# Performance work log

Hardware: AMD Instinct MI355X
Metric: run time of the kernel (lower is better)

## Reference

```python
import jax, jax.numpy as jnp
import numpy as np

D_MODEL = 128; N_HEADS = 4; N_LAYERS = 6
D_STATE = 16; D_CONV = 4; EXPAND = 2
D_INNER = EXPAND * D_MODEL          # 256
DT_RANK = (D_MODEL + 15) // 16      # 8
MLP_HID = 32
B, L = 8, 2048


def _ln(x, s, b):
    m = jnp.mean(x, -1, keepdims=True)
    v = jnp.var(x, -1, keepdims=True)
    return (x - m) / jnp.sqrt(v + 1e-5) * s + b


def _pe(length, d):
    # standard sinusoidal positional encoding [length, d]
    pos = jnp.arange(length, dtype=jnp.float32)[:, None]
    div = jnp.exp(jnp.arange(0, d, 2, dtype=jnp.float32) * (-np.log(10000.0) / d))
    pe = jnp.zeros((length, d), dtype=jnp.float32)
    pe = pe.at[:, 0::2].set(jnp.sin(pos * div))
    pe = pe.at[:, 1::2].set(jnp.cos(pos * div))
    return pe


def setup_inputs() -> dict:
    ks = iter(jax.random.split(jax.random.key(0), 48))
    def p(shape, scale=0.02):
        return jax.random.normal(next(ks), shape, dtype=jnp.float32) * scale
    return dict(
        x=jax.random.normal(next(ks), (B, L, 1), dtype=jnp.float32),
        mlp1_w=p((D_MODEL, 1)), mlp1_b=p((D_MODEL,)),
        qkv_w=p((N_LAYERS, 3 * D_MODEL, D_MODEL)), qkv_b=p((N_LAYERS, 3 * D_MODEL)),
        attn_out_w=p((N_LAYERS, D_MODEL, D_MODEL)), attn_out_b=p((N_LAYERS, D_MODEL)),
        ln1_s=jnp.ones((N_LAYERS, D_MODEL)), ln1_b=jnp.zeros((N_LAYERS, D_MODEL)),
        ffw_w1=p((N_LAYERS, D_MODEL, D_MODEL)), ffw_b1=p((N_LAYERS, D_MODEL)),
        ffw_w2=p((N_LAYERS, D_MODEL, D_MODEL)), ffw_b2=p((N_LAYERS, D_MODEL)),
        ln2_s=jnp.ones((N_LAYERS, D_MODEL)), ln2_b=jnp.zeros((N_LAYERS, D_MODEL)),
        in_proj_w=p((2 * D_INNER, D_MODEL)),
        conv_w=p((D_INNER, 1, D_CONV)), conv_b=p((D_INNER,)),
        x_proj_w=p((DT_RANK + 2 * D_STATE, D_INNER)),
        dt_proj_w=p((D_INNER, DT_RANK)), dt_proj_b=p((D_INNER,)),
        A_log=jnp.log(jnp.tile(jnp.arange(1, D_STATE + 1, dtype=jnp.float32), (D_INNER, 1))),
        D_skip=jnp.ones((D_INNER,), dtype=jnp.float32),
        out_proj_w=p((D_MODEL, D_INNER)),
        mlp2_w1=p((MLP_HID, D_MODEL)), mlp2_b1=p((MLP_HID,)),
        mlp2_w2=p((1, MLP_HID)), mlp2_b2=p((1,)),
    )


def _forward(x, mlp1_w, mlp1_b, qkv_w, qkv_b, attn_out_w, attn_out_b,
             ln1_s, ln1_b, ffw_w1, ffw_b1, ffw_w2, ffw_b2, ln2_s, ln2_b,
             in_proj_w, conv_w, conv_b, x_proj_w, dt_proj_w, dt_proj_b,
             A_log, D_skip, out_proj_w, mlp2_w1, mlp2_b1, mlp2_w2, mlp2_b2):
    b, l, _ = x.shape
    dh = D_MODEL // N_HEADS
    # mlp1 + positional encoding (dropout is identity at eval)
    h = x @ mlp1_w.T + mlp1_b                       # [B,L,D]
    h = h + _pe(l, D_MODEL)[None]
    # 6 post-norm self-attention + FFW layers (query_pos=None -> plain MHA)
    for i in range(N_LAYERS):
        qkv = h @ qkv_w[i].T + qkv_b[i]
        q, k, v = jnp.split(qkv, 3, axis=-1)
        q = q.reshape(b, l, N_HEADS, dh); k = k.reshape(b, l, N_HEADS, dh)
        v = v.reshape(b, l, N_HEADS, dh)
        scores = jnp.einsum('blhd,bmhd->bhlm', q, k) / jnp.sqrt(jnp.float32(dh))
        attn = jax.nn.softmax(scores, axis=-1)
        o = jnp.einsum('bhlm,bmhd->blhd', attn, v).reshape(b, l, D_MODEL)
        o = o @ attn_out_w[i].T + attn_out_b[i]
        h = _ln(h + o, ln1_s[i], ln1_b[i])
        f = jax.nn.relu(h @ ffw_w1[i].T + ffw_b1[i]) @ ffw_w2[i].T + ffw_b2[i]
        h = _ln(h + f, ln2_s[i], ln2_b[i])
    # Mamba block
    xz = h @ in_proj_w.T                            # [B,L,2*Din]
    xm, z = jnp.split(xz, 2, axis=-1)
    xc = xm.transpose(0, 2, 1)                      # [B,Din,L]
    xc = jax.lax.conv_general_dilated(
        xc, conv_w, (1,), [(D_CONV - 1, 0)],
        feature_group_count=D_INNER, dimension_numbers=('NCH', 'OIH', 'NCH'))
    xc = xc + conv_b[None, :, None]
    xm = jax.nn.silu(xc.transpose(0, 2, 1))         # [B,L,Din]
    dbc = xm @ x_proj_w.T                           # [B,L,dt_rank+2S]
    dt, Bm, Cm = jnp.split(dbc, [DT_RANK, DT_RANK + D_STATE], axis=-1)
    dt = jax.nn.softplus(dt @ dt_proj_w.T + dt_proj_b)  # [B,L,Din]
    A = -jnp.exp(A_log)                             # [Din,S]
    dA = jnp.exp(jnp.einsum('bld,ds->blds', dt, A))     # [B,L,Din,S]
    dBx = jnp.einsum('bld,bls,bld->blds', dt, Bm, xm)   # [B,L,Din,S]

    def step(hstate, inp):
        dA_t, dBx_t, C_t = inp
        hstate = hstate * dA_t + dBx_t             # [B,Din,S]
        y = jnp.einsum('bds,bs->bd', hstate, C_t)
        return hstate, y

    h0 = jnp.zeros((b, D_INNER, D_STATE), dtype=xm.dtype)
    _, ys = jax.lax.scan(step, h0, (dA.transpose(1, 0, 2, 3),
                                    dBx.transpose(1, 0, 2, 3),
                                    Cm.transpose(1, 0, 2)))
    y = ys.transpose(1, 0, 2)                       # [B,L,Din]
    y = y + xm * D_skip
    y = y * jax.nn.silu(z)
    y = y @ out_proj_w.T                            # [B,L,D]
    pooled = jnp.mean(y, axis=1)                    # [B,D]
    out = jax.nn.relu(pooled @ mlp2_w1.T + mlp2_b1) @ mlp2_w2.T + mlp2_b2
    return out                                      # [B,1]


def reference(x, mlp1_w, mlp1_b, qkv_w, qkv_b, attn_out_w, attn_out_b,
              ln1_s, ln1_b, ffw_w1, ffw_b1, ffw_w2, ffw_b2, ln2_s, ln2_b,
              in_proj_w, conv_w, conv_b, x_proj_w, dt_proj_w, dt_proj_b,
              A_log, D_skip, out_proj_w, mlp2_w1, mlp2_b1, mlp2_w2, mlp2_b2):
    return _forward(x, mlp1_w, mlp1_b, qkv_w, qkv_b, attn_out_w, attn_out_b,
                    ln1_s, ln1_b, ffw_w1, ffw_b1, ffw_w2, ffw_b2, ln2_s, ln2_b,
                    in_proj_w, conv_w, conv_b, x_proj_w, dt_proj_w, dt_proj_b,
                    A_log, D_skip, out_proj_w, mlp2_w1, mlp2_b1, mlp2_w2, mlp2_b2)
```

## Files before the change

### kernel.cpp

```cpp
#include <hip/hip_runtime.h>
#include <math.h>

#define BB 8
#define LL 2048
#define DMODEL 128
#define NHEAD 4
#define DHEAD 32
#define DIN 256
#define DSTATE 16
#define NLAYERS 6
#define BLROWS (BB*LL)
#define NCHUNK 32
#define CH 64

typedef __attribute__((ext_vector_type(8))) short short8;
typedef __attribute__((ext_vector_type(4))) float f32x4;

static __device__ __forceinline__ unsigned cvt_pk_bf16(float a, float b) {
    unsigned r;
    asm volatile("v_cvt_pk_bf16_f32 %0, %1, %2" : "=v"(r) : "v"(a), "v"(b));
    return r;
}
static __device__ __forceinline__ float fexp2(float x) {
    float r;
    asm("v_exp_f32 %0, %1" : "=v"(r) : "v"(x));
    return r;
}

__global__ __launch_bounds__(256) void wcvt_k(
    const float* __restrict__ src, ushort* __restrict__ dst, int n4)
{
    int i = blockIdx.x * 256 + threadIdx.x;
    if (i < n4) {
        float4 v = ((const float4*)src)[i];
        uint2 pw; pw.x = cvt_pk_bf16(v.x, v.y); pw.y = cvt_pk_bf16(v.z, v.w);
        ((uint2*)dst)[i] = pw;
    }
}

__global__ __launch_bounds__(256) void mlp1_pe_k(
    const float* __restrict__ x, const float* __restrict__ w,
    const float* __restrict__ b, float* __restrict__ h)
{
    int idx = blockIdx.x * 256 + threadIdx.x;
    int d   = idx & 127;
    int row = idx >> 7;
    int pos = row & (LL - 1);
    float v = x[row] * w[d] + b[d];
    int j2 = (d >> 1) * 2;
    float dv = expf((float)j2 * -0.07195578415603638f);
    float ang = (float)pos * dv;
    v += (d & 1) ? cosf(ang) : sinf(ang);
    h[idx] = v;
}

#define QSCALE (0.17677669529663687f * 1.4426950408889634f)
__global__ __launch_bounds__(256) void gemm_qkv_k(
    const float* __restrict__ A, const ushort* __restrict__ W16,
    const float* __restrict__ bias, ushort* __restrict__ C16)
{
    __shared__ __align__(16) short As[64][136];
    __shared__ __align__(16) short Ws[128][136];
    int tid = threadIdx.x;
    int w = tid >> 6, lane = tid & 63, lg = lane >> 4, lr = lane & 15;
    int row0 = blockIdx.y * 64, col0 = blockIdx.x * 128;

    const float* Ab = A + (size_t)row0 * 128;
    #pragma unroll
    for (int p = 0; p < 8; ++p) {
        int off = p * 1024 + tid * 4;
        float4 v = *(const float4*)(Ab + off);
        uint2 pw; pw.x = cvt_pk_bf16(v.x, v.y); pw.y = cvt_pk_bf16(v.z, v.w);
        *(uint2*)&As[off >> 7][off & 127] = pw;
    }
    const ushort* Wb = W16 + (size_t)col0 * 128;
    #pragma unroll
    for (int p = 0; p < 8; ++p) {
        int off = p * 2048 + tid * 8;
        short8 v = *(const short8*)(Wb + off);
        *(short8*)&Ws[off >> 7][off & 127] = v;
    }
    __syncthreads();

    short8 af[4];
    #pragma unroll
    for (int kk = 0; kk < 4; ++kk)
        af[kk] = *(short8*)&As[w * 16 + lr][kk * 32 + lg * 8];
    f32x4 acc[8];
    #pragma unroll
    for (int n = 0; n < 8; ++n) acc[n] = (f32x4){0.f, 0.f, 0.f, 0.f};
    #pragma unroll
    for (int n = 0; n < 8; ++n)
        #pragma unroll
        for (int kk = 0; kk < 4; ++kk) {
            short8 bf = *(short8*)&Ws[n * 16 + lr][kk * 32 + lg * 8];
            acc[n] = __builtin_amdgcn_mfma_f32_16x16x32_bf16(af[kk], bf, acc[n], 0, 0, 0);
        }
    float qs = (blockIdx.x == 0) ? QSCALE : 1.f;
    #pragma unroll
    for (int n = 0; n < 8; ++n) {
        int col = col0 + n * 16 + lr;
        float bv = bias[col];
        #pragma unroll
        for (int j = 0; j < 4; ++j) {
            int row = row0 + w * 16 + lg * 4 + j;
            float v = (acc[n][j] + bv) * qs;
            C16[(size_t)row * 384 + col] = (ushort)cvt_pk_bf16(v, v);
        }
    }
}

__global__ __launch_bounds__(256) void gemm_bf16_k(
    const float* __restrict__ A, const ushort* __restrict__ W16,
    float* __restrict__ C, int N)
{
    __shared__ __align__(16) short As[64][136];
    __shared__ __align__(16) short Ws[128][136];
    int tid = threadIdx.x;
    int w = tid >> 6, lane = tid & 63, lg = lane >> 4, lr = lane & 15;
    int row0 = blockIdx.y * 64, col0 = blockIdx.x * 128;

    const float* Ab = A + (size_t)row0 * 128;
    #pragma unroll
    for (int p = 0; p < 8; ++p) {
        int off = p * 1024 + tid * 4;
        float4 v = *(const float4*)(Ab + off);
        uint2 pw; pw.x = cvt_pk_bf16(v.x, v.y); pw.y = cvt_pk_bf16(v.z, v.w);
        *(uint2*)&As[off >> 7][off & 127] = pw;
    }
    const ushort* Wb = W16 + (size_t)col0 * 128;
    #pragma unroll
    for (int p = 0; p < 8; ++p) {
        int off = p * 2048 + tid * 8;
        short8 v = *(const short8*)(Wb + off);
        *(short8*)&Ws[off >> 7][off & 127] = v;
    }
    __syncthreads();

    short8 af[4];
    #pragma unroll
    for (int kk = 0; kk < 4; ++kk)
        af[kk] = *(short8*)&As[w * 16 + lr][kk * 32 + lg * 8];
    f32x4 acc[8];
    #pragma unroll
    for (int n = 0; n < 8; ++n) acc[n] = (f32x4){0.f, 0.f, 0.f, 0.f};
    #pragma unroll
    for (int n = 0; n < 8; ++n)
        #pragma unroll
        for (int kk = 0; kk < 4; ++kk) {
            short8 bf = *(short8*)&Ws[n * 16 + lr][kk * 32 + lg * 8];
            acc[n] = __builtin_amdgcn_mfma_f32_16x16x32_bf16(af[kk], bf, acc[n], 0, 0, 0);
        }
    #pragma unroll
    for (int n = 0; n < 8; ++n) {
        int col = col0 + n * 16 + lr;
        #pragma unroll
        for (int j = 0; j < 4; ++j) {
            int row = row0 + w * 16 + lg * 4 + j;
            C[(size_t)row * N + col] = acc[n][j];
        }
    }
}

__global__ __launch_bounds__(256) void gemm_ln_k(
    const ushort* __restrict__ A16, const ushort* __restrict__ W16,
    const float* __restrict__ bias, float* __restrict__ h,
    const float* __restrict__ ls, const float* __restrict__ lb)
{
    __shared__ __align__(16) short As[64][136];
    __shared__ __align__(16) short Ws[128][136];
    int tid = threadIdx.x;
    int w = tid >> 6, lane = tid & 63, lg = lane >> 4, lr = lane & 15;
    int row0 = blockIdx.x * 64;

    const ushort* Ab = A16 + (size_t)row0 * 128;
    #pragma unroll
    for (int p = 0; p < 4; ++p) {
        int off = p * 2048 + tid * 8;
        short8 v = *(const short8*)(Ab + off);
        *(short8*)&As[off >> 7][off & 127] = v;
    }
    #pragma unroll
    for (int p = 0; p < 8; ++p) {
        int off = p * 2048 + tid * 8;
        short8 v = *(const short8*)(W16 + off);
        *(short8*)&Ws[off >> 7][off & 127] = v;
    }
    __syncthreads();

    short8 af[4];
    #pragma unroll
    for (int kk = 0; kk < 4; ++kk)
        af[kk] = *(short8*)&As[w * 16 + lr][kk * 32 + lg * 8];
    f32x4 acc[8];
    #pragma unroll
    for (int n = 0; n < 8; ++n) acc[n] = (f32x4){0.f, 0.f, 0.f, 0.f};
    #pragma unroll
    for (int n = 0; n < 8; ++n)
        #pragma unroll
        for (int kk = 0; kk < 4; ++kk) {
            short8 bf = *(short8*)&Ws[n * 16 + lr][kk * 32 + lg * 8];
            acc[n] = __builtin_amdgcn_mfma_f32_16x16x32_bf16(af[kk], bf, acc[n], 0, 0, 0);
        }

    float bv[8], lsv[8], lbv[8];
    #pragma unroll
    for (int n = 0; n < 8; ++n) {
        int col = n * 16 + lr;
        bv[n] = bias[col]; lsv[n] = ls[col]; lbv[n] = lb[col];
    }
    #pragma unroll
    for (int j = 0; j < 4; ++j) {
        int row = row0 + w * 16 + lg * 4 + j;
        float xv[8]; float sum = 0.f;
        #pragma unroll
        for (int n = 0; n < 8; ++n) {
            xv[n] = acc[n][j] + bv[n] + h[(size_t)row * 128 + n * 16 + lr];
            sum += xv[n];
        }
        sum += __shfl_xor(sum, 1); sum += __shfl_xor(sum, 2);
        sum += __shfl_xor(sum, 4); sum += __shfl_xor(sum, 8);
        float mean = sum * (1.f / 128.f);
        float vs = 0.f;
        #pragma unroll
        for (int n = 0; n < 8; ++n) { float dd = xv[n] - mean; vs += dd * dd; }
        vs += __shfl_xor(vs, 1); vs += __shfl_xor(vs, 2);
        vs += __shfl_xor(vs, 4); vs += __shfl_xor(vs, 8);
        float inv = rsqrtf(vs * (1.f / 128.f) + 1e-5f);
        #pragma unroll
        for (int n = 0; n < 8; ++n)
            h[(size_t)row * 128 + n * 16 + lr] = (xv[n] - mean) * inv * lsv[n] + lbv[n];
    }
}

__global__ __launch_bounds__(256) void ffw_ln_k(
    float* __restrict__ h, const ushort* __restrict__ W1, const float* __restrict__ b1,
    const ushort* __restrict__ W2, const float* __restrict__ b2,
    const float* __restrict__ ls, const float* __restrict__ lb)
{
    __shared__ __align__(16) short As[64][136];
    __shared__ __align__(16) short Ws[128][136];
    int tid = threadIdx.x;
    int w = tid >> 6, lane = tid & 63, lg = lane >> 4, lr = lane & 15;
    int row0 = blockIdx.x * 64;

    const float* Ab = h + (size_t)row0 * 128;
    #pragma unroll
    for (int p = 0; p < 8; ++p) {
        int off = p * 1024 + tid * 4;
        float4 v = *(const float4*)(Ab + off);
        uint2 pw; pw.x = cvt_pk_bf16(v.x, v.y); pw.y = cvt_pk_bf16(v.z, v.w);
        *(uint2*)&As[off >> 7][off & 127] = pw;
    }
    #pragma unroll
    for (int p = 0; p < 8; ++p) {
        int off = p * 2048 + tid * 8;
        short8 v = *(const short8*)(W1 + off);
        *(short8*)&Ws[off >> 7][off & 127] = v;
    }
    __syncthreads();

    short8 af[4];
    #pragma unroll
    for (int kk = 0; kk < 4; ++kk)
        af[kk] = *(short8*)&As[w * 16 + lr][kk * 32 + lg * 8];
    f32x4 acc[8];
    #pragma unroll
    for (int n = 0; n < 8; ++n) acc[n] = (f32x4){0.f, 0.f, 0.f, 0.f};
    #pragma unroll
    for (int n = 0; n < 8; ++n)
        #pragma unroll
        for (int kk = 0; kk < 4; ++kk) {
            short8 bf = *(short8*)&Ws[n * 16 + lr][kk * 32 + lg * 8];
            acc[n] = __builtin_amdgcn_mfma_f32_16x16x32_bf16(af[kk], bf, acc[n], 0, 0, 0);
        }
    __syncthreads();

    {
        float b1v[8];
        #pragma unroll
        for (int n = 0; n < 8; ++n) b1v[n] = b1[n * 16 + lr];
        #pragma unroll
        for (int n = 0; n < 8; ++n) {
            #pragma unroll
            for (int j = 0; j < 4; ++j) {
                float hv = fmaxf(acc[n][j] + b1v[n], 0.f);
                As[w * 16 + lg * 4 + j][n * 16 + lr] = (short)cvt_pk_bf16(hv, hv);
            }
        }
    }
    #pragma unroll
    for (int p = 0; p < 8; ++p) {
        int off = p * 2048 + tid * 8;
        short8 v = *(const short8*)(W2 + off);
        *(short8*)&Ws[off >> 7][off & 127] = v;
    }
    __syncthreads();

    #pragma unroll
    for (int kk = 0; kk < 4; ++kk)
        af[kk] = *(short8*)&As[w * 16 + lr][kk * 32 + lg * 8];
    #pragma unroll
    for (int n = 0; n < 8; ++n) acc[n] = (f32x4){0.f, 0.f, 0.f, 0.f};
    #pragma unroll
    for (int n = 0; n < 8; ++n)
        #pragma unroll
        for (int kk = 0; kk < 4; ++kk) {
            short8 bf = *(short8*)&Ws[n * 16 + lr][kk * 32 + lg * 8];
            acc[n] = __builtin_amdgcn_mfma_f32_16x16x32_bf16(af[kk], bf, acc[n], 0, 0, 0);
        }

    float bv[8], lsv[8], lbv[8];
    #pragma unroll
    for (int n = 0; n < 8; ++n) {
        int col = n * 16 + lr;
        bv[n] = b2[col]; lsv[n] = ls[col]; lbv[n] = lb[col];
    }
    #pragma unroll
    for (int j = 0; j < 4; ++j) {
        int row = row0 + w * 16 + lg * 4 + j;
        float xv[8]; float sum = 0.f;
        #pragma unroll
        for (int n = 0; n < 8; ++n) {
            xv[n] = acc[n][j] + bv[n] + h[(size_t)row * 128 + n * 16 + lr];
            sum += xv[n];
        }
        sum += __shfl_xor(sum, 1); sum += __shfl_xor(sum, 2);
        sum += __shfl_xor(sum, 4); sum += __shfl_xor(sum, 8);
        float mean = sum * (1.f / 128.f);
        float vs = 0.f;
        #pragma unroll
        for (int n = 0; n < 8; ++n) { float dd = xv[n] - mean; vs += dd * dd; }
        vs += __shfl_xor(vs, 1); vs += __shfl_xor(vs, 2);
        vs += __shfl_xor(vs, 4); vs += __shfl_xor(vs, 8);
        float inv = rsqrtf(vs * (1.f / 128.f) + 1e-5f);
        #pragma unroll
        for (int n = 0; n < 8; ++n)
            h[(size_t)row * 128 + n * 16 + lr] = (xv[n] - mean) * inv * lsv[n] + lbv[n];
    }
}

__global__ __launch_bounds__(256) void attn_mfma_k(
    const ushort* __restrict__ qkv, ushort* __restrict__ o)
{
    __shared__ __align__(16) char smem[16384];

    int bid = blockIdx.x;
    int b  = bid & 7;
    int qt = (bid >> 3) & 15;
    int hd = bid >> 7;
    int tid  = threadIdx.x;
    int wave = tid >> 6;
    int lane = tid & 63;
    int lg = lane >> 4, lr = lane & 15;

    const ushort* base = qkv + (size_t)b * LL * 384;
    int qr0 = qt * 128 + wave * 32;

    short8 qfA = *(const short8*)(base + (size_t)(qr0 + lr) * 384 + hd * 32 + lg * 8);
    short8 qfB = *(const short8*)(base + (size_t)(qr0 + 16 + lr) * 384 + hd * 32 + lg * 8);

    int kk = tid >> 2, ks = tid & 3;
    int krow = kk & 31;
    int kchk = (((kk >> 5) << 2) + ks) ^ (krow & 7);
    int kwo = krow * 128 + (kchk << 4);
    const ushort* kptr = base + (size_t)kk * 384 + 128 + hd * 32 + ks * 8;

    int k2 = (tid & 31) * 2, d0 = (tid >> 5) * 4;
    int rl = k2 & 31;
    int colp = (k2 >> 5) * 32 + ((rl >> 2) & 3) * 8 + (rl >> 4) * 4 + (rl & 3);
    int vchunk = colp >> 3;
    int vinb   = (colp * 2) & 15;
    int vwo0 = (d0+0)*128 + (((vchunk ^ ((d0+0)&7)) << 4) | vinb);
    int vwo1 = (d0+1)*128 + (((vchunk ^ ((d0+1)&7)) << 4) | vinb);
    int vwo2 = (d0+2)*128 + (((vchunk ^ ((d0+2)&7)) << 4) | vinb);
    int vwo3 = (d0+3)*128 + (((vchunk ^ ((d0+3)&7)) << 4) | vinb);
    const ushort* vptr = base + (size_t)k2 * 384 + 256 + hd * 32 + d0;

    int kro[4];
    #pragma unroll
    for (int n = 0; n < 4; ++n) {
        int r = ((n & 1) << 4) + lr;
        int c = (((n >> 1) << 2) + lg) ^ (r & 7);
        kro[n] = r * 128 + (c << 4);
    }
    int sx = (lg ^ (lr & 7)) << 4;
    int sy = ((4 + lg) ^ (lr & 7)) << 4;
    int vro0 = lr * 128 + sx;
    int vro1 = (16 + lr) * 128 + sx;
    int vro2 = lr * 128 + sy;
    int vro3 = (16 + lr) * 128 + sy;

    f32x4 OfA[2] = {}, OfB[2] = {};
    f32x4 OlA = {}, OlB = {};
    const f32x4 zero4 = {0.f, 0.f, 0.f, 0.f};
    short8 ones;
    #pragma unroll
    for (int e = 0; e < 8; ++e) ones[e] = (short)0x3F80;

    const int TSTR = 64 * 384;
    const ushort* knext = kptr;
    const ushort* vnext = vptr;

    {
        short8 kreg = *(const short8*)knext;
        uint2 va = *(const uint2*)vnext;
        uint2 vb = *(const uint2*)(vnext + 384);
        knext += TSTR; vnext += TSTR;
        *(short8*)(smem + 0 + kwo) = kreg;
        uint w0 = (va.x & 0xFFFFu) | (vb.x << 16);
        uint w1 = (va.x >> 16)     | (vb.x & 0xFFFF0000u);
        uint w2 = (va.y & 0xFFFFu) | (vb.y << 16);
        uint w3 = (va.y >> 16)     | (vb.y & 0xFFFF0000u);
        *(uint*)(smem + 8192 + vwo0) = w0;
        *(uint*)(smem + 8192 + vwo1) = w1;
        *(uint*)(smem + 8192 + vwo2) = w2;
        *(uint*)(smem + 8192 + vwo3) = w3;
    }
    __syncthreads();

#define ATTN_TILE(KRB, VRB, KWB, VWB, LAST) do {                              \
    short8 kreg_; uint2 va_, vb_;                                             \
    if (!(LAST)) {                                                            \
        kreg_ = *(const short8*)knext;                                        \
        va_   = *(const uint2*)vnext;                                         \
        vb_   = *(const uint2*)(vnext + 384);                                 \
        knext += TSTR; vnext += TSTR;                                         \
    }                                                                         \
    short8 kf0_ = *(const short8*)(smem + (KRB) + kro[0]);                    \
    short8 kf1_ = *(const short8*)(smem + (KRB) + kro[1]);                    \
    short8 kf2_ = *(const short8*)(smem + (KRB) + kro[2]);                    \
    short8 kf3_ = *(const short8*)(smem + (KRB) + kro[3]);                    \
    f32x4 SA0_ = __builtin_amdgcn_mfma_f32_16x16x32_bf16(kf0_, qfA, zero4,0,0,0); \
    f32x4 SA1_ = __builtin_amdgcn_mfma_f32_16x16x32_bf16(kf1_, qfA, zero4,0,0,0); \
    f32x4 SA2_ = __builtin_amdgcn_mfma_f32_16x16x32_bf16(kf2_, qfA, zero4,0,0,0); \
    f32x4 SA3_ = __builtin_amdgcn_mfma_f32_16x16x32_bf16(kf3_, qfA, zero4,0,0,0); \
    f32x4 SB0_ = __builtin_amdgcn_mfma_f32_16x16x32_bf16(kf0_, qfB, zero4,0,0,0); \
    f32x4 SB1_ = __builtin_amdgcn_mfma_f32_16x16x32_bf16(kf1_, qfB, zero4,0,0,0); \
    f32x4 SB2_ = __builtin_amdgcn_mfma_f32_16x16x32_bf16(kf2_, qfB, zero4,0,0,0); \
    f32x4 SB3_ = __builtin_amdgcn_mfma_f32_16x16x32_bf16(kf3_, qfB, zero4,0,0,0); \
    union { uint4 u; short8 s; } paA0_, paA1_, paB0_, paB1_;                  \
    paA0_.u.x = cvt_pk_bf16(fexp2(SA0_[0]), fexp2(SA0_[1]));                  \
    paA0_.u.y = cvt_pk_bf16(fexp2(SA0_[2]), fexp2(SA0_[3]));                  \
    paA0_.u.z = cvt_pk_bf16(fexp2(SA1_[0]), fexp2(SA1_[1]));                  \
    paA0_.u.w = cvt_pk_bf16(fexp2(SA1_[2]), fexp2(SA1_[3]));                  \
    paA1_.u.x = cvt_pk_bf16(fexp2(SA2_[0]), fexp2(SA2_[1]));                  \
    paA1_.u.y = cvt_pk_bf16(fexp2(SA2_[2]), fexp2(SA2_[3]));                  \
    paA1_.u.z = cvt_pk_bf16(fexp2(SA3_[0]), fexp2(SA3_[1]));                  \
    paA1_.u.w = cvt_pk_bf16(fexp2(SA3_[2]), fexp2(SA3_[3]));                  \
    paB0_.u.x = cvt_pk_bf16(fexp2(SB0_[0]), fexp2(SB0_[1]));                  \
    paB0_.u.y = cvt_pk_bf16(fexp2(SB0_[2]), fexp2(SB0_[3]));                  \
    paB0_.u.z = cvt_pk_bf16(fexp2(SB1_[0]), fexp2(SB1_[1]));                  \
    paB0_.u.w = cvt_pk_bf16(fexp2(SB1_[2]), fexp2(SB1_[3]));                  \
    paB1_.u.x = cvt_pk_bf16(fexp2(SB2_[0]), fexp2(SB2_[1]));                  \
    paB1_.u.y = cvt_pk_bf16(fexp2(SB2_[2]), fexp2(SB2_[3]));                  \
    paB1_.u.z = cvt_pk_bf16(fexp2(SB3_[0]), fexp2(SB3_[1]));                  \
    paB1_.u.w = cvt_pk_bf16(fexp2(SB3_[2]), fexp2(SB3_[3]));                  \
    short8 vb00_ = *(const short8*)(smem + (VRB) + vro0);                     \
    short8 vb01_ = *(const short8*)(smem + (VRB) + vro1);                     \
    short8 vb10_ = *(const short8*)(smem + (VRB) + vro2);                     \
    short8 vb11_ = *(const short8*)(smem + (VRB) + vro3);                     \
    OlA    = __builtin_amdgcn_mfma_f32_16x16x32_bf16(paA0_.s, ones,  OlA,   0,0,0); \
    OfA[0] = __builtin_amdgcn_mfma_f32_16x16x32_bf16(paA0_.s, vb00_, OfA[0],0,0,0); \
    OfA[1] = __builtin_amdgcn_mfma_f32_16x16x32_bf16(paA0_.s, vb01_, OfA[1],0,0,0); \
    OlA    = __builtin_amdgcn_mfma_f32_16x16x32_bf16(paA1_.s, ones,  OlA,   0,0,0); \
    OfA[0] = __builtin_amdgcn_mfma_f32_16x16x32_bf16(paA1_.s, vb10_, OfA[0],0,0,0); \
    OfA[1] = __builtin_amdgcn_mfma_f32_16x16x32_bf16(paA1_.s, vb11_, OfA[1],0,0,0); \
    OlB    = __builtin_amdgcn_mfma_f32_16x16x32_bf16(paB0_.s, ones,  OlB,   0,0,0); \
    OfB[0] = __builtin_amdgcn_mfma_f32_16x16x32_bf16(paB0_.s, vb00_, OfB[0],0,0,0); \
    OfB[1] = __builtin_amdgcn_mfma_f32_16x16x32_bf16(paB0_.s, vb01_, OfB[1],0,0,0); \
    OlB    = __builtin_amdgcn_mfma_f32_16x16x32_bf16(paB1_.s, ones,  OlB,   0,0,0); \
    OfB[0] = __builtin_amdgcn_mfma_f32_16x16x32_bf16(paB1_.s, vb10_, OfB[0],0,0,0); \
    OfB[1] = __builtin_amdgcn_mfma_f32_16x16x32_bf16(paB1_.s, vb11_, OfB[1],0,0,0); \
    if (!(LAST)) {                                                            \
        *(short8*)(smem + (KWB) + kwo) = kreg_;                               \
        uint w0_ = (va_.x & 0xFFFFu) | (vb_.x << 16);                         \
        uint w1_ = (va_.x >> 16)     | (vb_.x & 0xFFFF0000u);                 \
        uint w2_ = (va_.y & 0xFFFFu) | (vb_.y << 16);                         \
        uint w3_ = (va_.y >> 16)     | (vb_.y & 0xFFFF0000u);                 \
        *(uint*)(smem + (VWB) + vwo0) = w0_;                                  \
        *(uint*)(smem + (VWB) + vwo1) = w1_;                                  \
        *(uint*)(smem + (VWB) + vwo2) = w2_;                                  \
        *(uint*)(smem + (VWB) + vwo3) = w3_;                                  \
    }                                                                         \
    __syncthreads();                                                          \
} while (0)

    #pragma unroll 1
    for (int t = 0; t < 32; t += 2) {
        ATTN_TILE(0,    8192,  4096, 12288, false);
        ATTN_TILE(4096, 12288, 0,    8192,  (t + 2 >= 32));
    }
#undef ATTN_TILE

    #pragma unroll
    for (int j = 0; j < 4; ++j) {
        float invA = 1.f / OlA[j];
        int qA = qr0 + lg * 4 + j;
        size_t obA = ((size_t)b * LL + qA) * DMODEL + hd * 32;
        float a0 = OfA[0][j] * invA, a1 = OfA[1][j] * invA;
        o[obA + lr]      = (ushort)cvt_pk_bf16(a0, a0);
        o[obA + 16 + lr] = (ushort)cvt_pk_bf16(a1, a1);
        float invB = 1.f / OlB[j];
        int qB = qr0 + 16 + lg * 4 + j;
        size_t obB = ((size_t)b * LL + qB) * DMODEL + hd * 32;
        float b0 = OfB[0][j] * invB, b1 = OfB[1][j] * invB;
        o[obB + lr]      = (ushort)cvt_pk_bf16(b0, b0);
        o[obB + 16 + lr] = (ushort)cvt_pk_bf16(b1, b1);
    }
}

__global__ __launch_bounds__(256) void xproj_bf16_k(
    const float* __restrict__ A, const ushort* __restrict__ W16,
    float* __restrict__ C)
{
    __shared__ __align__(16) short As[64][264];
    __shared__ __align__(16) short Ws[48][264];
    int tid = threadIdx.x;
    int w = tid >> 6, lane = tid & 63, lg = lane >> 4, lr = lane & 15;
    int row0 = blockIdx.x * 64;

    const float* Ab = A + (size_t)row0 * 256;
    #pragma unroll
    for (int p = 0; p < 16; ++p) {
        int off = p * 1024 + tid * 4;
        float4 v = *(const float4*)(Ab + off);
        uint2 pw; pw.x = cvt_pk_bf16(v.x, v.y); pw.y = cvt_pk_bf16(v.z, v.w);
        *(uint2*)&As[off >> 8][off & 255] = pw;
    }
    #pragma unroll
    for (int p = 0; p < 6; ++p) {
        int off = p * 2048 + tid * 8;
        int r = off >> 8, c = off & 255;
        short8 v = {};
        if (r < 40) v = *(const short8*)(W16 + (size_t)r * 256 + c);
        *(short8*)&Ws[r][c] = v;
    }
    __syncthreads();

    short8 af[8];
    #pragma unroll
    for (int kk = 0; kk < 8; ++kk)
        af[kk] = *(short8*)&As[w * 16 + lr][kk * 32 + lg * 8];

    f32x4 acc[3];
    #pragma unroll
    for (int n = 0; n < 3; ++n) acc[n] = (f32x4){0.f, 0.f, 0.f, 0.f};
    #pragma unroll
    for (int n = 0; n < 3; ++n)
        #pragma unroll
        for (int kk = 0; kk < 8; ++kk) {
            short8 bf = *(short8*)&Ws[n * 16 + lr][kk * 32 + lg * 8];
            acc[n] = __builtin_amdgcn_mfma_f32_16x16x32_bf16(af[kk], bf, acc[n], 0, 0, 0);
        }
    #pragma unroll
    for (int n = 0; n < 3; ++n) {
        int col = n * 16 + lr;
        if (col < 40) {
            #pragma unroll
            for (int j = 0; j < 4; ++j) {
                int row = row0 + w * 16 + lg * 4 + j;
                C[(size_t)row * 40 + col] = acc[n][j];
            }
        }
    }
}

__global__ __launch_bounds__(256) void conv_silu_k(
    const float* __restrict__ xz, const float* __restrict__ cw,
    const float* __restrict__ cb, float* __restrict__ xm)
{
    int idx = blockIdx.x * 256 + threadIdx.x;
    int d   = idx & 255;
    int row = idx >> 8;
    int l   = row & (LL - 1);
    float a = cb[d];
    #pragma unroll
    for (int t = 0; t < 4; ++t) {
        int ll = l - 3 + t;
        if (ll >= 0) a += cw[d * 4 + t] * xz[(size_t)(row - 3 + t) * 512 + d];
    }
    float sg = 1.f / (1.f + expf(-a));
    xm[idx] = a * sg;
}

__global__ __launch_bounds__(256) void dtproj_k(
    const float* __restrict__ dbc, const float* __restrict__ w,
    const float* __restrict__ bias, float* __restrict__ dt)
{
    int row0 = blockIdx.x * 4, n = threadIdx.x;
    __shared__ float dv[4][8];
    if (n < 32) dv[n >> 3][n & 7] = dbc[(size_t)(row0 + (n >> 3)) * 40 + (n & 7)];
    __syncthreads();
    float bv = bias[n];
    float wv[8];
    #pragma unroll
    for (int k = 0; k < 8; ++k) wv[k] = w[n * 8 + k];
    #pragma unroll
    for (int r = 0; r < 4; ++r) {
        float a = bv;
        #pragma unroll
        for (int k = 0; k < 8; ++k) a += dv[r][k] * wv[k];
        float sp = fmaxf(a, 0.f) + log1pf(expf(-fabsf(a)));
        dt[(size_t)(row0 + r) * 256 + n] = sp;
    }
}

__global__ __launch_bounds__(512) void scan1_k(
    const float* __restrict__ dt, const float* __restrict__ xm,
    const float* __restrict__ dbc, const float* __restrict__ A_log,
    float* __restrict__ Asum, float* __restrict__ Bsum)
{
    int blk = blockIdx.x;
    int c = blk & 31, b = blk >> 5;
    int tid = threadIdx.x;
    int d = tid >> 1, sh = tid & 1;
    float Av2[8];
    {
        float4 a0 = *(const float4*)(A_log + d * 16 + sh * 8);
        float4 a1 = *(const float4*)(A_log + d * 16 + sh * 8 + 4);
        Av2[0] = -expf(a0.x) * 1.4426950408889634f;
        Av2[1] = -expf(a0.y) * 1.4426950408889634f;
        Av2[2] = -expf(a0.z) * 1.4426950408889634f;
        Av2[3] = -expf(a0.w) * 1.4426950408889634f;
        Av2[4] = -expf(a1.x) * 1.4426950408889634f;
        Av2[5] = -expf(a1.y) * 1.4426950408889634f;
        Av2[6] = -expf(a1.z) * 1.4426950408889634f;
        Av2[7] = -expf(a1.w) * 1.4426950408889634f;
    }
    float aarg[8] = {}, Bacc[8] = {};
    __shared__ float Bst[CH][16];
    size_t rowb = (size_t)b * LL + c * CH;
    {
        int e = tid * 2;
        int j = e >> 4, col = e & 15;
        float2 v = *(const float2*)(dbc + (rowb + j) * 40 + 8 + col);
        Bst[j][col] = v.x; Bst[j][col + 1] = v.y;
    }
    __syncthreads();
    #pragma unroll 4
    for (int j = 0; j < CH; ++j) {
        size_t rr = rowb + j;
        float dtv = dt[rr * 256 + d];
        float xmv = xm[rr * 256 + d];
        float dtxm = dtv * xmv;
        float4 b0 = *(const float4*)&Bst[j][sh * 8];
        float4 b1 = *(const float4*)&Bst[j][sh * 8 + 4];
        float bb[8] = {b0.x, b0.y, b0.z, b0.w, b1.x, b1.y, b1.z, b1.w};
        #pragma unroll
        for (int k = 0; k < 8; ++k) {
            float arg = dtv * Av2[k];
            Bacc[k] = Bacc[k] * fexp2(arg) + bb[k] * dtxm;
            aarg[k] += arg;
        }
    }
    #pragma unroll
    for (int k = 0; k < 8; ++k) {
        size_t oo = ((size_t)(blk * 16 + sh * 8 + k)) * 256 + d;
        Asum[oo] = fexp2(aarg[k]);
        Bsum[oo] = Bacc[k];
    }
}

__global__ __launch_bounds__(256) void scan_mid_k(
    const float* __restrict__ Asum, const float* __restrict__ Bsum,
    float* __restrict__ hinit)
{
    int b = blockIdx.x >> 4, s = blockIdx.x & 15;
    int d = threadIdx.x;
    float h = 0.f;
    #pragma unroll 4
    for (int c = 0; c < NCHUNK; ++c) {
        size_t oo = ((size_t)((b * 32 + c) * 16 + s)) * 256 + d;
        hinit[oo] = h;
        h = Asum[oo] * h + Bsum[oo];
    }
}

__global__ __launch_bounds__(512) void scan2_k(
    const float* __restrict__ dt, const float* __restrict__ xm,
    const float* __restrict__ dbc, const float* __restrict__ A_log,
    const float* __restrict__ hinit, const float* __restrict__ xz,
    const float* __restrict__ dsk, float* __restrict__ part)
{
    int blk = blockIdx.x;
    int c = blk & 31, b = blk >> 5;
    int tid = threadIdx.x;
    int d = tid >> 1, sh = tid & 1;
    float Av2[8];
    {
        float4 a0 = *(const float4*)(A_log + d * 16 + sh * 8);
        float4 a1 = *(const float4*)(A_log + d * 16 + sh * 8 + 4);
        Av2[0] = -expf(a0.x) * 1.4426950408889634f;
        Av2[1] = -expf(a0.y) * 1.4426950408889634f;
        Av2[2] = -expf(a0.z) * 1.4426950408889634f;
        Av2[3] = -expf(a0.w) * 1.4426950408889634f;
        Av2[4] = -expf(a1.x) * 1.4426950408889634f;
        Av2[5] = -expf(a1.y) * 1.4426950408889634f;
        Av2[6] = -expf(a1.z) * 1.4426950408889634f;
        Av2[7] = -expf(a1.w) * 1.4426950408889634f;
    }
    float hs[8];
    #pragma unroll
    for (int k = 0; k < 8; ++k)
        hs[k] = hinit[((size_t)(blk * 16 + sh * 8 + k)) * 256 + d];
    float dskv = dsk[d];
    float psum = 0.f;
    __shared__ float Bst[CH][16], Cst[CH][16];
    size_t rowb = (size_t)b * LL + c * CH;
    {
        int e = tid * 2;
        int j = e >> 4, col = e & 15;
        float2 v = *(const float2*)(dbc + (rowb + j) * 40 + 8 + col);
        Bst[j][col] = v.x; Bst[j][col + 1] = v.y;
        float2 u = *(const float2*)(dbc + (rowb + j) * 40 + 24 + col);
        Cst[j][col] = u.x; Cst[j][col + 1] = u.y;
    }
    __syncthreads();
    #pragma unroll 2
    for (int j = 0; j < CH; ++j) {
        size_t rr = rowb + j;
        float dtv = dt[rr * 256 + d];
        float xmv = xm[rr * 256 + d];
        float dtxm = dtv * xmv;
        float4 b0 = *(const float4*)&Bst[j][sh * 8];
        float4 b1 = *(const float4*)&Bst[j][sh * 8 + 4];
        float4 c0 = *(const float4*)&Cst[j][sh * 8];
        float4 c1 = *(const float4*)&Cst[j][sh * 8 + 4];
        float bb[8] = {b0.x, b0.y, b0.z, b0.w, b1.x, b1.y, b1.z, b1.w};
        float cc[8] = {c0.x, c0.y, c0.z, c0.w, c1.x, c1.y, c1.z, c1.w};
        float yv = 0.f;
        #pragma unroll
        for (int k = 0; k < 8; ++k) {
            float dA = fexp2(dtv * Av2[k]);
            hs[k] = hs[k] * dA + bb[k] * dtxm;
            yv += hs[k] * cc[k];
        }
        yv += __shfl_xor(yv, 1);
        float zv = xz[rr * 512 + 256 + d];
        float sg = zv / (1.f + __expf(-zv));
        psum += (yv + xmv * dskv) * sg;
    }
    if (sh == 0) part[(size_t)blk * 256 + d] = psum;
}

__global__ __launch_bounds__(128) void final_k(
    const float* __restrict__ part, const float* __restrict__ opw,
    const float* __restrict__ w1, const float* __restrict__ b1,
    const float* __restrict__ w2, const float* __restrict__ b2,
    float* __restrict__ out)
{
    int b = blockIdx.x, t = threadIdx.x;
    __shared__ float pg[256];
    __shared__ float pooled[128];
    __shared__ float hid[32];
    for (int k = t; k < 256; k += 128) {
        float sm = 0.f;
        #pragma unroll
        for (int c = 0; c < NCHUNK; ++c)
            sm += part[(size_t)(b * 32 + c) * 256 + k];
        pg[k] = sm * (1.f / 2048.f);
    }
    __syncthreads();
    float a = 0.f;
    for (int k = 0; k < 256; ++k) a += pg[k] * opw[(size_t)t * DIN + k];
    pooled[t] = a;
    __syncthreads();
    if (t < 32) {
        float hh = b1[t];
        for (int d2 = 0; d2 < 128; ++d2) hh += pooled[d2] * w1[t * 128 + d2];
        hid[t] = fmaxf(hh, 0.f);
    }
    __syncthreads();
    if (t == 0) {
        float o = b2[0];
        #pragma unroll
        for (int j = 0; j < 32; ++j) o += hid[j] * w2[j];
        out[b] = o;
    }
}

extern "C" void kernel_launch(void* const* d_in, const int* in_sizes, int n_in,
                              void* d_out, int out_size, void* d_ws, size_t ws_size,
                              hipStream_t stream)
{
    const float* x          = (const float*)d_in[0];
    const float* mlp1_w     = (const float*)d_in[1];
    const float* mlp1_b     = (const float*)d_in[2];
    const float* qkv_w      = (const float*)d_in[3];
    const float* qkv_b      = (const float*)d_in[4];
    const float* attn_out_w = (const float*)d_in[5];
    const float* attn_out_b = (const float*)d_in[6];
    const float* ln1_s      = (const float*)d_in[7];
    const float* ln1_b      = (const float*)d_in[8];
    const float* ffw_w1     = (const float*)d_in[9];
    const float* ffw_b1     = (const float*)d_in[10];
    const float* ffw_w2     = (const float*)d_in[11];
    const float* ffw_b2     = (const float*)d_in[12];
    const float* ln2_s      = (const float*)d_in[13];
    const float* ln2_b      = (const float*)d_in[14];
    const float* in_proj_w  = (const float*)d_in[15];
    const float* conv_w     = (const float*)d_in[16];
    const float* conv_b     = (const float*)d_in[17];
    const float* x_proj_w   = (const float*)d_in[18];
    const float* dt_proj_w  = (const float*)d_in[19];
    const float* dt_proj_b  = (const float*)d_in[20];
    const float* A_log      = (const float*)d_in[21];
    const float* D_skip     = (const float*)d_in[22];
    const float* out_proj_w = (const float*)d_in[23];
    const float* mlp2_w1    = (const float*)d_in[24];
    const float* mlp2_b1    = (const float*)d_in[25];
    const float* mlp2_w2    = (const float*)d_in[26];
    const float* mlp2_b2    = (const float*)d_in[27];
    float* out = (float*)d_out;
    float* ws  = (float*)d_ws;

    float* h     = ws;
    float* xz    = h    + (size_t)BLROWS * DMODEL;
    float* t1    = xz   + (size_t)BLROWS * 512;
    float* t2    = t1   + (size_t)BLROWS * DMODEL;
    float* xm    = t2   + (size_t)BLROWS * DMODEL;
    float* dbc   = xm   + (size_t)BLROWS * DIN;
    float* part2 = dbc  + (size_t)BLROWS * 40;
    float* Asum  = part2 + 8 * 32 * 256;
    float* Bsum  = Asum + 8 * 32 * 16 * 256;
    float* hini  = Bsum + 8 * 32 * 16 * 256;
    ushort* w16  = (ushort*)(hini + 8 * 32 * 16 * 256);
    ushort* qkvw16 = w16;
    ushort* aow16  = w16 + 294912;
    ushort* f1w16  = w16 + 393216;
    ushort* f2w16  = w16 + 491520;
    ushort* ipw16  = w16 + 589824;
    ushort* xpw16  = w16 + 655360;
    ushort* qkv16 = (ushort*)xz;
    ushort* t1u   = (ushort*)t1;
    float* dtb  = t1;
    (void)t2;

    wcvt_k<<<(294912/4 + 255)/256, 256, 0, stream>>>(qkv_w, qkvw16, 294912/4);
    wcvt_k<<<(98304/4 + 255)/256, 256, 0, stream>>>(attn_out_w, aow16, 98304/4);
    wcvt_k<<<(98304/4 + 255)/256, 256, 0, stream>>>(ffw_w1, f1w16, 98304/4);
    wcvt_k<<<(98304/4 + 255)/256, 256, 0, stream>>>(ffw_w2, f2w16, 98304/4);
    wcvt_k<<<(65536/4 + 255)/256, 256, 0, stream>>>(in_proj_w, ipw16, 65536/4);
    wcvt_k<<<(10240/4 + 255)/256, 256, 0, stream>>>(x_proj_w, xpw16, 10240/4);

    mlp1_pe_k<<<(BLROWS * DMODEL) / 256, 256, 0, stream>>>(x, mlp1_w, mlp1_b, h);

    for (int i = 0; i < NLAYERS; ++i) {
        gemm_qkv_k<<<dim3(3, 256), 256, 0, stream>>>(
            h, qkvw16 + (size_t)i * 384 * 128, qkv_b + i * 384, qkv16);
        attn_mfma_k<<<512, 256, 0, stream>>>(qkv16, t1u);
        gemm_ln_k<<<256, 256, 0, stream>>>(
            t1u, aow16 + (size_t)i * 128 * 128, attn_out_b + i * 128, h,
            ln1_s + i * 128, ln1_b + i * 128);
        ffw_ln_k<<<256, 256, 0, stream>>>(
            h, f1w16 + (size_t)i * 128 * 128, ffw_b1 + i * 128,
            f2w16 + (size_t)i * 128 * 128, ffw_b2 + i * 128,
            ln2_s + i * 128, ln2_b + i * 128);
    }

    gemm_bf16_k<<<dim3(4, 256), 256, 0, stream>>>(h, ipw16, xz, 512);
    conv_silu_k<<<(BLROWS * DIN) / 256, 256, 0, stream>>>(xz, conv_w, conv_b, xm);
    xproj_bf16_k<<<256, 256, 0, stream>>>(xm, xpw16, dbc);
    dtproj_k<<<BLROWS / 4, 256, 0, stream>>>(dbc, dt_proj_w, dt_proj_b, dtb);
    scan1_k<<<256, 512, 0, stream>>>(dtb, xm, dbc, A_log, Asum, Bsum);
    scan_mid_k<<<128, 256, 0, stream>>>(Asum, Bsum, hini);
    scan2_k<<<256, 512, 0, stream>>>(dtb, xm, dbc, A_log, hini, xz, D_skip, part2);
    final_k<<<8, 128, 0, stream>>>(part2, out_proj_w, mlp2_w1, mlp2_b1, mlp2_w2, mlp2_b2, out);
}
```

Baseline: 468.3 us.

## Split attention over two key halves with a separate merge kernel

Result: slower. 480.6 us (+2.6%).

```diff
diff --git a/kernel.cpp b/kernel.cpp
--- a/kernel.cpp
+++ b/kernel.cpp
@@ -340,15 +340,17 @@
     }
 }
 
-__global__ __launch_bounds__(256) void attn_mfma_k(
-    const ushort* __restrict__ qkv, ushort* __restrict__ o)
+__global__ __launch_bounds__(256) void attn_part_k(
+    const ushort* __restrict__ qkv, float* __restrict__ Opart,
+    float* __restrict__ lpart)
 {
     __shared__ __align__(16) char smem[16384];
 
     int bid = blockIdx.x;
-    int b  = bid & 7;
-    int qt = (bid >> 3) & 15;
-    int hd = bid >> 7;
+    int b    = bid & 7;
+    int qt   = (bid >> 3) & 15;
+    int hd   = (bid >> 7) & 3;
+    int half = bid >> 9;
     int tid  = threadIdx.x;
     int wave = tid >> 6;
     int lane = tid & 63;
@@ -364,7 +366,7 @@
     int krow = kk & 31;
     int kchk = (((kk >> 5) << 2) + ks) ^ (krow & 7);
     int kwo = krow * 128 + (kchk << 4);
-    const ushort* kptr = base + (size_t)kk * 384 + 128 + hd * 32 + ks * 8;
+    const ushort* kptr = base + (size_t)(half * 1024 + kk) * 384 + 128 + hd * 32 + ks * 8;
 
     int k2 = (tid & 31) * 2, d0 = (tid >> 5) * 4;
     int rl = k2 & 31;
@@ -375,7 +377,7 @@
     int vwo1 = (d0+1)*128 + (((vchunk ^ ((d0+1)&7)) << 4) | vinb);
     int vwo2 = (d0+2)*128 + (((vchunk ^ ((d0+2)&7)) << 4) | vinb);
     int vwo3 = (d0+3)*128 + (((vchunk ^ ((d0+3)&7)) << 4) | vinb);
-    const ushort* vptr = base + (size_t)k2 * 384 + 256 + hd * 32 + d0;
+    const ushort* vptr = base + (size_t)(half * 1024 + k2) * 384 + 256 + hd * 32 + d0;
 
     int kro[4];
     #pragma unroll
@@ -487,27 +489,47 @@
 } while (0)
 
     #pragma unroll 1
-    for (int t = 0; t < 32; t += 2) {
+    for (int t = 0; t < 16; t += 2) {
         ATTN_TILE(0,    8192,  4096, 12288, false);
-        ATTN_TILE(4096, 12288, 0,    8192,  (t + 2 >= 32));
+        ATTN_TILE(4096, 12288, 0,    8192,  (t + 2 >= 16));
     }
 #undef ATTN_TILE
 
     #pragma unroll
     for (int j = 0; j < 4; ++j) {
-        float invA = 1.f / OlA[j];
-        int qA = qr0 + lg * 4 + j;
-        size_t obA = ((size_t)b * LL + qA) * DMODEL + hd * 32;
-        float a0 = OfA[0][j] * invA, a1 = OfA[1][j] * invA;
-        o[obA + lr]      = (ushort)cvt_pk_bf16(a0, a0);
-        o[obA + 16 + lr] = (ushort)cvt_pk_bf16(a1, a1);
-        float invB = 1.f / OlB[j];
-        int qB = qr0 + 16 + lg * 4 + j;
-        size_t obB = ((size_t)b * LL + qB) * DMODEL + hd * 32;
-        float b0 = OfB[0][j] * invB, b1 = OfB[1][j] * invB;
-        o[obB + lr]      = (ushort)cvt_pk_bf16(b0, b0);
-        o[obB + 16 + lr] = (ushort)cvt_pk_bf16(b1, b1);
-    }
+        int qa = wave * 32 + lg * 4 + j;
+        size_t oa = ((size_t)bid * 128 + qa) * 32;
+        Opart[oa + lr]      = OfA[0][j];
+        Opart[oa + 16 + lr] = OfA[1][j];
+        if (lr == 0) lpart[(size_t)bid * 128 + qa] = OlA[j];
+        int qb = qa + 16;
+        size_t ob = ((size_t)bid * 128 + qb) * 32;
+        Opart[ob + lr]      = OfB[0][j];
+        Opart[ob + 16 + lr] = OfB[1][j];
+        if (lr == 0) lpart[(size_t)bid * 128 + qb] = OlB[j];
+    }
+}
+
+__global__ __launch_bounds__(256) void attn_merge_k(
+    const float* __restrict__ Opart, const float* __restrict__ lpart,
+    ushort* __restrict__ o)
+{
+    int i = blockIdx.x * 256 + threadIdx.x;
+    int d2  = (i & 63) * 2;
+    int row = i >> 6;
+    int b = row >> 11, q = row & 2047;
+    int hd = d2 >> 5, dl = d2 & 31;
+    int qt = q >> 7, ql = q & 127;
+    int bid0 = (hd << 7) | (qt << 3) | b;
+    int bid1 = bid0 + 512;
+    size_t p0 = ((size_t)bid0 * 128 + ql) * 32 + dl;
+    size_t p1 = ((size_t)bid1 * 128 + ql) * 32 + dl;
+    float2 a = *(const float2*)(Opart + p0);
+    float2 c = *(const float2*)(Opart + p1);
+    float l = lpart[(size_t)bid0 * 128 + ql] + lpart[(size_t)bid1 * 128 + ql];
+    float inv = 1.f / l;
+    unsigned pw = cvt_pk_bf16((a.x + c.x) * inv, (a.y + c.y) * inv);
+    *(unsigned*)(o + (size_t)row * 128 + d2) = pw;
 }
 
 __global__ __launch_bounds__(256) void xproj_bf16_k(
@@ -835,6 +857,8 @@
     ushort* qkv16 = (ushort*)xz;
     ushort* t1u   = (ushort*)t1;
     float* dtb  = t1;
+    float* Oprt = xm;
+    float* lprt = dbc;
     (void)t2;
 
     wcvt_k<<<(294912/4 + 255)/256, 256, 0, stream>>>(qkv_w, qkvw16, 294912/4);
@@ -849,7 +873,8 @@
     for (int i = 0; i < NLAYERS; ++i) {
         gemm_qkv_k<<<dim3(3, 256), 256, 0, stream>>>(
             h, qkvw16 + (size_t)i * 384 * 128, qkv_b + i * 384, qkv16);
-        attn_mfma_k<<<512, 256, 0, stream>>>(qkv16, t1u);
+        attn_part_k<<<1024, 256, 0, stream>>>(qkv16, Oprt, lprt);
+        attn_merge_k<<<(BLROWS * 64) / 256, 256, 0, stream>>>(Oprt, lprt, t1u);
         gemm_ln_k<<<256, 256, 0, stream>>>(
             t1u, aow16 + (size_t)i * 128 * 128, attn_out_b + i * 128, h,
             ln1_s + i * 128, ln1_b + i * 128);
```

## Write V in pre-interleaved row-pair layout from QKV GEMM; add MFMA priority

Applied to the files above, without the earlier changes.

Result: no change. 459.7 us (-1.8%).

```diff
diff --git a/kernel.cpp b/kernel.cpp
--- a/kernel.cpp
+++ b/kernel.cpp
@@ -57,7 +57,8 @@
 #define QSCALE (0.17677669529663687f * 1.4426950408889634f)
 __global__ __launch_bounds__(256) void gemm_qkv_k(
     const float* __restrict__ A, const ushort* __restrict__ W16,
-    const float* __restrict__ bias, ushort* __restrict__ C16)
+    const float* __restrict__ bias, ushort* __restrict__ C16,
+    unsigned* __restrict__ vbuf)
 {
     __shared__ __align__(16) short As[64][136];
     __shared__ __align__(16) short Ws[128][136];
@@ -96,16 +97,33 @@
             short8 bf = *(short8*)&Ws[n * 16 + lr][kk * 32 + lg * 8];
             acc[n] = __builtin_amdgcn_mfma_f32_16x16x32_bf16(af[kk], bf, acc[n], 0, 0, 0);
         }
-    float qs = (blockIdx.x == 0) ? QSCALE : 1.f;
-    #pragma unroll
-    for (int n = 0; n < 8; ++n) {
-        int col = col0 + n * 16 + lr;
-        float bv = bias[col];
-        #pragma unroll
-        for (int j = 0; j < 4; ++j) {
-            int row = row0 + w * 16 + lg * 4 + j;
-            float v = (acc[n][j] + bv) * qs;
-            C16[(size_t)row * 384 + col] = (ushort)cvt_pk_bf16(v, v);
+
+    if (blockIdx.x == 2) {
+        #pragma unroll
+        for (int n = 0; n < 8; ++n) {
+            int dfull = n * 16 + lr;
+            int hd2 = dfull >> 5, dl = dfull & 31;
+            float bv = bias[256 + dfull];
+            #pragma unroll
+            for (int p = 0; p < 2; ++p) {
+                int row = row0 + w * 16 + lg * 4 + p * 2;
+                int bb2 = row >> 11, l = row & 2047;
+                unsigned pw = cvt_pk_bf16(acc[n][p * 2] + bv, acc[n][p * 2 + 1] + bv);
+                vbuf[(((size_t)bb2 * 4 + hd2) * 1024 + (l >> 1)) * 32 + dl] = pw;
+            }
+        }
+    } else {
+        float qs = (blockIdx.x == 0) ? QSCALE : 1.f;
+        #pragma unroll
+        for (int n = 0; n < 8; ++n) {
+            int col = col0 + n * 16 + lr;
+            float bv = bias[col];
+            #pragma unroll
+            for (int j = 0; j < 4; ++j) {
+                int row = row0 + w * 16 + lg * 4 + j;
+                float v = (acc[n][j] + bv) * qs;
+                C16[(size_t)row * 384 + col] = (ushort)cvt_pk_bf16(v, v);
+            }
         }
     }
 }
@@ -341,7 +359,8 @@
 }
 
 __global__ __launch_bounds__(256) void attn_mfma_k(
-    const ushort* __restrict__ qkv, ushort* __restrict__ o)
+    const ushort* __restrict__ qkv, const unsigned* __restrict__ vbuf,
+    ushort* __restrict__ o)
 {
     __shared__ __align__(16) char smem[16384];
 
@@ -375,7 +394,7 @@
     int vwo1 = (d0+1)*128 + (((vchunk ^ ((d0+1)&7)) << 4) | vinb);
     int vwo2 = (d0+2)*128 + (((vchunk ^ ((d0+2)&7)) << 4) | vinb);
     int vwo3 = (d0+3)*128 + (((vchunk ^ ((d0+3)&7)) << 4) | vinb);
-    const ushort* vptr = base + (size_t)k2 * 384 + 256 + hd * 32 + d0;
+    const unsigned* vptr = vbuf + (((size_t)b * 4 + hd) * 1024 + (k2 >> 1)) * 32 + d0;
 
     int kro[4];
     #pragma unroll
@@ -399,38 +418,34 @@
     for (int e = 0; e < 8; ++e) ones[e] = (short)0x3F80;
 
     const int TSTR = 64 * 384;
+    const int VSTR = 32 * 32;
     const ushort* knext = kptr;
-    const ushort* vnext = vptr;
+    const unsigned* vnext = vptr;
 
     {
         short8 kreg = *(const short8*)knext;
-        uint2 va = *(const uint2*)vnext;
-        uint2 vb = *(const uint2*)(vnext + 384);
-        knext += TSTR; vnext += TSTR;
+        uint4 vv = *(const uint4*)vnext;
+        knext += TSTR; vnext += VSTR;
         *(short8*)(smem + 0 + kwo) = kreg;
-        uint w0 = (va.x & 0xFFFFu) | (vb.x << 16);
-        uint w1 = (va.x >> 16)     | (vb.x & 0xFFFF0000u);
-        uint w2 = (va.y & 0xFFFFu) | (vb.y << 16);
-        uint w3 = (va.y >> 16)     | (vb.y & 0xFFFF0000u);
-        *(uint*)(smem + 8192 + vwo0) = w0;
-        *(uint*)(smem + 8192 + vwo1) = w1;
-        *(uint*)(smem + 8192 + vwo2) = w2;
-        *(uint*)(smem + 8192 + vwo3) = w3;
+        *(unsigned*)(smem + 8192 + vwo0) = vv.x;
+        *(unsigned*)(smem + 8192 + vwo1) = vv.y;
+        *(unsigned*)(smem + 8192 + vwo2) = vv.z;
+        *(unsigned*)(smem + 8192 + vwo3) = vv.w;
     }
     __syncthreads();
 
 #define ATTN_TILE(KRB, VRB, KWB, VWB, LAST) do {                              \
-    short8 kreg_; uint2 va_, vb_;                                             \
+    short8 kreg_; uint4 vv_;                                                  \
     if (!(LAST)) {                                                            \
         kreg_ = *(const short8*)knext;                                        \
-        va_   = *(const uint2*)vnext;                                         \
-        vb_   = *(const uint2*)(vnext + 384);                                 \
-        knext += TSTR; vnext += TSTR;                                         \
+        vv_   = *(const uint4*)vnext;                                         \
+        knext += TSTR; vnext += VSTR;                                         \
     }                                                                         \
     short8 kf0_ = *(const short8*)(smem + (KRB) + kro[0]);                    \
     short8 kf1_ = *(const short8*)(smem + (KRB) + kro[1]);                    \
     short8 kf2_ = *(const short8*)(smem + (KRB) + kro[2]);                    \
     short8 kf3_ = *(const short8*)(smem + (KRB) + kro[3]);                    \
+    __builtin_amdgcn_s_setprio(1);                                            \
     f32x4 SA0_ = __builtin_amdgcn_mfma_f32_16x16x32_bf16(kf0_, qfA, zero4,0,0,0); \
     f32x4 SA1_ = __builtin_amdgcn_mfma_f32_16x16x32_bf16(kf1_, qfA, zero4,0,0,0); \
     f32x4 SA2_ = __builtin_amdgcn_mfma_f32_16x16x32_bf16(kf2_, qfA, zero4,0,0,0); \
@@ -472,16 +487,13 @@
     OlB    = __builtin_amdgcn_mfma_f32_16x16x32_bf16(paB1_.s, ones,  OlB,   0,0,0); \
     OfB[0] = __builtin_amdgcn_mfma_f32_16x16x32_bf16(paB1_.s, vb10_, OfB[0],0,0,0); \
     OfB[1] = __builtin_amdgcn_mfma_f32_16x16x32_bf16(paB1_.s, vb11_, OfB[1],0,0,0); \
+    __builtin_amdgcn_s_setprio(0);                                            \
     if (!(LAST)) {                                                            \
         *(short8*)(smem + (KWB) + kwo) = kreg_;                               \
-        uint w0_ = (va_.x & 0xFFFFu) | (vb_.x << 16);                         \
-        uint w1_ = (va_.x >> 16)     | (vb_.x & 0xFFFF0000u);                 \
-        uint w2_ = (va_.y & 0xFFFFu) | (vb_.y << 16);                         \
-        uint w3_ = (va_.y >> 16)     | (vb_.y & 0xFFFF0000u);                 \
-        *(uint*)(smem + (VWB) + vwo0) = w0_;                                  \
-        *(uint*)(smem + (VWB) + vwo1) = w1_;                                  \
-        *(uint*)(smem + (VWB) + vwo2) = w2_;                                  \
-        *(uint*)(smem + (VWB) + vwo3) = w3_;                                  \
+        *(unsigned*)(smem + (VWB) + vwo0) = vv_.x;                            \
+        *(unsigned*)(smem + (VWB) + vwo1) = vv_.y;                            \
+        *(unsigned*)(smem + (VWB) + vwo2) = vv_.z;                            \
+        *(unsigned*)(smem + (VWB) + vwo3) = vv_.w;                            \
     }                                                                         \
     __syncthreads();                                                          \
 } while (0)
@@ -832,6 +844,7 @@
     ushort* f2w16  = w16 + 491520;
     ushort* ipw16  = w16 + 589824;
     ushort* xpw16  = w16 + 655360;
+    unsigned* vbuf = (unsigned*)(w16 + 665600);
     ushort* qkv16 = (ushort*)xz;
     ushort* t1u   = (ushort*)t1;
     float* dtb  = t1;
@@ -848,8 +861,8 @@
 
     for (int i = 0; i < NLAYERS; ++i) {
         gemm_qkv_k<<<dim3(3, 256), 256, 0, stream>>>(
-            h, qkvw16 + (size_t)i * 384 * 128, qkv_b + i * 384, qkv16);
-        attn_mfma_k<<<512, 256, 0, stream>>>(qkv16, t1u);
+            h, qkvw16 + (size_t)i * 384 * 128, qkv_b + i * 384, qkv16, vbuf);
+        attn_mfma_k<<<512, 256, 0, stream>>>(qkv16, vbuf, t1u);
         gemm_ln_k<<<256, 256, 0, stream>>>(
             t1u, aow16 + (size_t)i * 128 * 128, attn_out_b + i * 128, h,
             ln1_s + i * 128, ln1_b + i * 128);
```
